# Performance work log

Measured on AMD Instinct MI355X. Metric: run time of the kernel, lower is better.

The kernel has to match this reference:

```python
import jax, jax.numpy as jnp
import numpy as np

DIM = 128        # per-head dim == model width in this module
Q_HEADS = 16
KV_HEADS = 4
WINDOW = 512
BATCH = 4
SEQ = 2048


def setup_inputs() -> dict:
    key = jax.random.key(0)
    k1, k2, k3 = jax.random.split(key, 3)
    x = jax.random.normal(k1, (BATCH, SEQ, DIM), dtype=jnp.float32)
    # fused qkv weight, stored (in, out) so forward is x @ W_qkv
    W_qkv = jax.random.normal(k2, (DIM, (Q_HEADS + 2 * KV_HEADS) * DIM), dtype=jnp.float32) * (DIM ** -0.5)
    W_proj = jax.random.normal(k3, (Q_HEADS * DIM, DIM), dtype=jnp.float32) * ((Q_HEADS * DIM) ** -0.5)
    return {"x": x, "W_qkv": W_qkv, "W_proj": W_proj}


def _gqa_forward(x, W_qkv, W_proj):
    b, s, d = x.shape
    qkv = x @ W_qkv                                    # [b, s, (Hq+2Hkv)*d]
    qkv = qkv.reshape(b, s, Q_HEADS + 2 * KV_HEADS, d).transpose(0, 2, 1, 3)
    q = qkv[:, :Q_HEADS]                               # [b, Hq, s, d]
    k = qkv[:, Q_HEADS:Q_HEADS + KV_HEADS]             # [b, Hkv, s, d]
    v = qkv[:, Q_HEADS + KV_HEADS:]                    # [b, Hkv, s, d]

    # GQA: repeat kv heads to match q heads
    group = Q_HEADS // KV_HEADS
    k = jnp.repeat(k, group, axis=1)                   # [b, Hq, s, d]
    v = jnp.repeat(v, group, axis=1)

    scale = 1.0 / jnp.sqrt(jnp.float32(d))
    scores = jnp.einsum('bhqd,bhkd->bhqk', q, k) * scale   # [b, Hq, s, s]

    q_idx = jnp.arange(s)[:, None]
    kv_idx = jnp.arange(s)[None, :]
    rel = (q_idx - kv_idx).astype(jnp.float32)         # [s, s]
    # per-head ALiBi slope: exp2(-(h+1)*8/Hq), added (sign matches source)
    h = jnp.arange(Q_HEADS, dtype=jnp.float32)
    slopes = jnp.exp2(-((h + 1.0) * 8.0 / Q_HEADS))    # [Hq]
    scores = scores + slopes[None, :, None, None] * rel[None, None, :, :]

    mask = (q_idx >= kv_idx) & ((q_idx - kv_idx) <= WINDOW)
    scores = jnp.where(mask[None, None], scores, -jnp.inf)
    probs = jax.nn.softmax(scores, axis=-1)

    att = jnp.einsum('bhqk,bhkd->bhqd', probs, v)      # [b, Hq, s, d]
    att = att.transpose(0, 2, 1, 3).reshape(b, s, Q_HEADS * d)
    return att @ W_proj                                # [b, s, d]


def reference(x, W_qkv, W_proj):
    return _gqa_forward(x, W_qkv, W_proj)
```

## Files before the change

kernel.cpp:

```cpp
#include <hip/hip_runtime.h>
#include <math.h>

#define DIM_    128
#define QH_     16
#define KVH_    4
#define WIN_    512
#define BATCH_  4
#define SEQ_    2048
#define QKV_LD  3072
#define ATT_LD  2048

#define NX   (BATCH_*SEQ_*DIM_)
#define NWQ  (DIM_*QKV_LD)
#define NWP  (ATT_LD*DIM_)

typedef __attribute__((ext_vector_type(8))) short short8;
typedef __attribute__((ext_vector_type(4))) float f32x4;
typedef unsigned short u16;
typedef unsigned int u32;

__device__ __forceinline__ u16 f2bf(float f) {
    u32 u = __float_as_uint(f);
    u += 0x7fff + ((u >> 16) & 1);
    return (u16)(u >> 16);
}
__device__ __forceinline__ float bf2f(u16 u) {
    return __uint_as_float(((u32)u) << 16);
}
#define MFMA16 __builtin_amdgcn_mfma_f32_16x16x32_bf16

#if __has_builtin(__builtin_amdgcn_exp2f)
#define EXP2F __builtin_amdgcn_exp2f
#else
#define EXP2F exp2f
#endif

__device__ __forceinline__ void gload_lds16(const u16* g, u16* l) {
    __builtin_amdgcn_global_load_lds(
        (const __attribute__((address_space(1))) unsigned int*)(const void*)g,
        (__attribute__((address_space(3))) unsigned int*)(void*)l, 16, 0, 0);
}

__global__ __launch_bounds__(256) void prep(
    const float* __restrict__ x, const float* __restrict__ Wqkv,
    const float* __restrict__ Wproj,
    u16* __restrict__ xh, u16* __restrict__ wth, u16* __restrict__ wpth)
{
    if (blockIdx.x < 1024) {
        const size_t t = (size_t)blockIdx.x * 256 + threadIdx.x;
        float4 v = *(const float4*)(x + 4 * t);
        ushort4 o;
        o.x = f2bf(v.x); o.y = f2bf(v.y); o.z = f2bf(v.z); o.w = f2bf(v.w);
        *(ushort4*)(xh + 4 * t) = o;
        return;
    }
    __shared__ float T[32][33];
    int tile = blockIdx.x - 1024;
    const float* src; u16* dst; int K, N;
    if (tile < 384) { src = Wqkv;  dst = wth;  K = 128;  N = 3072; }
    else { tile -= 384; src = Wproj; dst = wpth; K = 2048; N = 128; }
    const int ntile = N >> 5;
    const int k0 = (tile / ntile) << 5, n0 = (tile % ntile) << 5;
    const int tx = threadIdx.x & 31, ty = threadIdx.x >> 5;
    #pragma unroll
    for (int i = 0; i < 4; ++i)
        T[ty + 8 * i][tx] = src[(size_t)(k0 + ty + 8 * i) * N + n0 + tx];
    __syncthreads();
    #pragma unroll
    for (int i = 0; i < 4; ++i)
        dst[(size_t)(n0 + ty + 8 * i) * K + k0 + tx] = f2bf(T[tx][ty + 8 * i]);
}

__global__ __launch_bounds__(256) void gemm1_mfma(
    const u16* __restrict__ xh, const u16* __restrict__ wth,
    u16* __restrict__ qkvb, u16* __restrict__ vg)
{
    __shared__ u16 Ab[32][512];
    __shared__ u16 Bb[16][512];
    const int bn = blockIdx.x * 64;
    const int bm = blockIdx.y * 128;
    const int tid = threadIdx.x;
    const int wv = tid >> 6, lane = tid & 63;
    const int lr = lane & 15, quad = lane >> 4;
    const int lo = lane & 15, hi = lane >> 4;

    #pragma unroll
    for (int i = 0; i < 12; ++i) {
        const int idx = wv * 12 + i;
        if (idx < 32) {
            const int mt = idx >> 2, s = idx & 3;
            gload_lds16(xh + (size_t)(bm + mt * 16 + lo) * DIM_ + s * 32 + hi * 8,
                        &Ab[idx][0]);
        } else {
            const int j = idx - 32, nt = j >> 2, s = j & 3;
            gload_lds16(wth + (size_t)(bn + nt * 16 + lo) * DIM_ + s * 32 + hi * 8,
                        &Bb[j][0]);
        }
    }
    __syncthreads();

    const int wr = wv >> 1, wc = wv & 1;
    f32x4 acc[4][2] = {};
    if (bn < 2560) {
        #pragma unroll
        for (int s = 0; s < 4; ++s) {
            short8 af[4], bf[2];
            #pragma unroll
            for (int mt = 0; mt < 4; ++mt)
                af[mt] = *(const short8*)&Ab[(wr * 4 + mt) * 4 + s][lane * 8];
            #pragma unroll
            for (int nt = 0; nt < 2; ++nt)
                bf[nt] = *(const short8*)&Bb[(wc * 2 + nt) * 4 + s][lane * 8];
            #pragma unroll
            for (int mt = 0; mt < 4; ++mt)
                #pragma unroll
                for (int nt = 0; nt < 2; ++nt)
                    acc[mt][nt] = MFMA16(bf[nt], af[mt], acc[mt][nt], 0, 0, 0);
        }
        #pragma unroll
        for (int mt = 0; mt < 4; ++mt)
            #pragma unroll
            for (int nt = 0; nt < 2; ++nt) {
                ushort4 o;
                o.x = f2bf(acc[mt][nt][0]); o.y = f2bf(acc[mt][nt][1]);
                o.z = f2bf(acc[mt][nt][2]); o.w = f2bf(acc[mt][nt][3]);
                *(ushort4*)(qkvb
                    + (size_t)(bm + wr * 64 + mt * 16 + lr) * QKV_LD
                    + bn + wc * 32 + nt * 16 + quad * 4) = o;
            }
    } else {
        #pragma unroll
        for (int s = 0; s < 4; ++s) {
            short8 af[4], bf[2];
            #pragma unroll
            for (int mt = 0; mt < 4; ++mt)
                af[mt] = *(const short8*)&Ab[(wr * 4 + mt) * 4 + s][lane * 8];
            #pragma unroll
            for (int nt = 0; nt < 2; ++nt)
                bf[nt] = *(const short8*)&Bb[(wc * 2 + nt) * 4 + s][lane * 8];
            #pragma unroll
            for (int mt = 0; mt < 4; ++mt)
                #pragma unroll
                for (int nt = 0; nt < 2; ++nt)
                    acc[mt][nt] = MFMA16(af[mt], bf[nt], acc[mt][nt], 0, 0, 0);
        }
        #pragma unroll
        for (int mt = 0; mt < 4; ++mt)
            #pragma unroll
            for (int nt = 0; nt < 2; ++nt) {
                const int ncol = bn + wc * 32 + nt * 16 + lr - 2560;
                const int kvh = ncol >> 7, d = ncol & 127;
                const int m0 = bm + wr * 64 + mt * 16 + quad * 4;
                ushort4 o;
                o.x = f2bf(acc[mt][nt][0]); o.y = f2bf(acc[mt][nt][1]);
                o.z = f2bf(acc[mt][nt][2]); o.w = f2bf(acc[mt][nt][3]);
                *(ushort4*)(vg + ((size_t)((m0 >> 11) * KVH_ + kvh) * DIM_ + d)
                            * SEQ_ + (m0 & 2047)) = o;
            }
    }
}

__global__ __launch_bounds__(256) void attn_mfma(
    const u16* __restrict__ qkvb, const u16* __restrict__ vg,
    u16* __restrict__ ah)
{
    const int xcd  = blockIdx.x & 7;
    const int idx  = blockIdx.x >> 3;
    const int pair = xcd + 8 * (idx & 1);
    const int qt   = idx >> 1;
    const int b    = pair >> 2, kvh = pair & 3;
    const int q0 = qt << 5;
    const int tid = threadIdx.x;
    const int wv = tid >> 6, lane = tid & 63;
    const int lr = lane & 15, quad = lane >> 4;
    const int h = kvh * 4 + wv;

    __shared__ u16 Kb[4][8][512];
    __shared__ u16 Vb[4][8][512];
    __shared__ u16 Pt[4][32][36];

    const float scale2 = 0.08838834764831845f * 1.4426950408889634f;
    const float slope2 = exp2f(-0.5f * (float)(h + 1)) * 1.4426950408889634f;
    const int jbase = max(0, q0 - WIN_);
    const int nch = (q0 + 32 - jbase) >> 5;
    const size_t rowb = (size_t)b * SEQ_;
    const u16* kg  = qkvb + rowb * QKV_LD + (QH_ + kvh) * DIM_;
    const u16* vgb = vg + (size_t)(b * KVH_ + kvh) * DIM_ * SEQ_;
    const int lo = lane & 15, hi = lane >> 4;

    short8 qf[2][4];
    #pragma unroll
    for (int m = 0; m < 2; ++m) {
        const u16* qp = qkvb + (rowb + q0 + m * 16 + lr) * QKV_LD
                        + h * DIM_ + quad * 8;
        #pragma unroll
        for (int s = 0; s < 4; ++s) qf[m][s] = *(const short8*)(qp + 32 * s);
    }

    float alpha[2];
    #pragma unroll
    for (int m = 0; m < 2; ++m) {
        const int q = q0 + m * 16 + lr;
        const int rm = (q < WIN_) ? q : WIN_;
        alpha[m] = slope2 * (float)(q - rm);
    }

    f32x4 O[2][8] = {};
    float rs[2] = {0.f, 0.f};

    #define STAGE(CH, SLOT) do {                                              \
        const int _jk = jbase + ((CH) << 5);                                  \
        _Pragma("unroll")                                                     \
        for (int _t = 0; _t < 2; ++_t) {                                      \
            const int _p = wv + _t * 4;                                       \
            gload_lds16(kg + (size_t)(_jk + (_p >> 2) * 16 + lo) * QKV_LD     \
                        + (_p & 3) * 32 + hi * 8, &Kb[(SLOT)][_p][0]);        \
            gload_lds16(vgb + (size_t)(_p * 16 + lo) * SEQ_ + _jk + hi * 8,   \
                        &Vb[(SLOT)][_p][0]);                                  \
        }                                                                     \
    } while (0)

    STAGE(0, 0);
    { const int c1 = (1 < nch) ? 1 : (nch - 1); STAGE(c1, 1); }

    for (int ch = 0; ch < nch; ++ch) {
        const int jk = jbase + (ch << 5);
        const int slot = ch & 3;
        { const int cn = (ch + 2 < nch) ? (ch + 2) : (nch - 1);
          STAGE(cn, (ch + 2) & 3); }
        __asm__ volatile("s_waitcnt vmcnt(8)" ::: "memory");
        __asm__ volatile("s_barrier" ::: "memory");

        #pragma unroll
        for (int nt = 0; nt < 2; ++nt) {
            f32x4 c0 = {0.f, 0.f, 0.f, 0.f}, c1 = {0.f, 0.f, 0.f, 0.f};
            #pragma unroll
            for (int s = 0; s < 4; ++s) {
                short8 kf = *(const short8*)&Kb[slot][nt * 4 + s][lane * 8];
                c0 = MFMA16(kf, qf[0][s], c0, 0, 0, 0);
                c1 = MFMA16(kf, qf[1][s], c1, 0, 0, 0);
            }
            const int jknt = jk + nt * 16;
            #pragma unroll
            for (int m = 0; m < 2; ++m) {
                const f32x4 c = m ? c1 : c0;
                const int qm0 = q0 + m * 16;
                const float b0 = fmaf(-slope2, (float)(jknt + quad * 4), alpha[m]);
                float e0, e1, e2, e3;
                if (qm0 >= jknt + 15 && qm0 + 15 <= jknt + WIN_) {
                    e0 = EXP2F(fmaf(c[0], scale2, b0));
                    e1 = EXP2F(fmaf(c[1], scale2, b0 - slope2));
                    e2 = EXP2F(fmaf(c[2], scale2, b0 - 2.f * slope2));
                    e3 = EXP2F(fmaf(c[3], scale2, b0 - 3.f * slope2));
                } else {
                    const int q = qm0 + lr, j0q = jknt + quad * 4;
                    float ee[4];
                    #pragma unroll
                    for (int r = 0; r < 4; ++r) {
                        const int rel = q - (j0q + r);
                        const float t = fmaf(c[r], scale2, b0 - (float)r * slope2);
                        ee[r] = ((unsigned)rel <= (unsigned)WIN_) ? EXP2F(t) : 0.f;
                    }
                    e0 = ee[0]; e1 = ee[1]; e2 = ee[2]; e3 = ee[3];
                }
                rs[m] += (e0 + e1) + (e2 + e3);
                ushort4 o;
                o.x = f2bf(e0); o.y = f2bf(e1); o.z = f2bf(e2); o.w = f2bf(e3);
                *(ushort4*)&Pt[wv][m * 16 + lr][nt * 16 + quad * 4] = o;
            }
        }
        __asm__ volatile("s_waitcnt lgkmcnt(0)" ::: "memory");

        short8 pa0 = *(const short8*)&Pt[wv][lr][quad * 8];
        short8 pa1 = *(const short8*)&Pt[wv][16 + lr][quad * 8];
        #pragma unroll
        for (int nt = 0; nt < 8; ++nt) {
            short8 vf = *(const short8*)&Vb[slot][nt][lane * 8];
            O[0][nt] = MFMA16(vf, pa0, O[0][nt], 0, 0, 0);
            O[1][nt] = MFMA16(vf, pa1, O[1][nt], 0, 0, 0);
        }
    }
    #undef STAGE

    __asm__ volatile("s_waitcnt vmcnt(0)" ::: "memory");

    #pragma unroll
    for (int m = 0; m < 2; ++m) {
        rs[m] += __shfl_xor(rs[m], 16);
        rs[m] += __shfl_xor(rs[m], 32);
    }

    #pragma unroll
    for (int m = 0; m < 2; ++m) {
        const float inv = 1.0f / rs[m];
        u16* dst = ah + (rowb + q0 + m * 16 + lr) * (size_t)ATT_LD + h * DIM_;
        #pragma unroll
        for (int nt = 0; nt < 8; ++nt) {
            ushort4 o;
            o.x = f2bf(O[m][nt][0] * inv); o.y = f2bf(O[m][nt][1] * inv);
            o.z = f2bf(O[m][nt][2] * inv); o.w = f2bf(O[m][nt][3] * inv);
            *(ushort4*)(dst + nt * 16 + quad * 4) = o;
        }
    }
}

__global__ __launch_bounds__(256) void gemm2_mfma(
    const u16* __restrict__ ah, const u16* __restrict__ wpth,
    float* __restrict__ out)
{
    const int bm = blockIdx.x * 16;
    const int wv = threadIdx.x >> 6, lane = threadIdx.x & 63;
    const int lr = lane & 15, quad = lane >> 4;
    const int cq = wv;

    const u16* arow  = ah + (size_t)(bm + lr) * ATT_LD + quad * 8;
    const u16* w0row = wpth + (size_t)(cq * 32 + lr) * ATT_LD + quad * 8;
    const u16* w1row = w0row + (size_t)16 * ATT_LD;

    f32x4 acc0 = {0.f, 0.f, 0.f, 0.f}, acc1 = {0.f, 0.f, 0.f, 0.f};
    #pragma unroll 8
    for (int k0 = 0; k0 < ATT_LD; k0 += 32) {
        short8 a  = *(const short8*)(arow + k0);
        short8 w0 = *(const short8*)(w0row + k0);
        short8 w1 = *(const short8*)(w1row + k0);
        acc0 = MFMA16(w0, a, acc0, 0, 0, 0);
        acc1 = MFMA16(w1, a, acc1, 0, 0, 0);
    }
    float* orow = out + (size_t)(bm + lr) * DIM_ + cq * 32;
    *(float4*)(orow + quad * 4)      = *(float4*)&acc0;
    *(float4*)(orow + 16 + quad * 4) = *(float4*)&acc1;
}

extern "C" void kernel_launch(void* const* d_in, const int* in_sizes, int n_in,
                              void* d_out, int out_size, void* d_ws, size_t ws_size,
                              hipStream_t stream)
{
    const float* x     = (const float*)d_in[0];
    const float* Wqkv  = (const float*)d_in[1];
    const float* Wproj = (const float*)d_in[2];
    float* out = (float*)d_out;

    u16* xh   = (u16*)d_ws;
    u16* wth  = xh   + (size_t)NX;
    u16* wpth = wth  + (size_t)NWQ;
    u16* qkvb = wpth + (size_t)NWP;
    u16* vg   = qkvb + (size_t)8192 * QKV_LD;
    u16* ahp  = vg   + (size_t)BATCH_ * KVH_ * DIM_ * SEQ_;

    prep<<<1024 + 640, 256, 0, stream>>>(x, Wqkv, Wproj, xh, wth, wpth);

    gemm1_mfma<<<dim3(QKV_LD / 64, 8192 / 128), 256, 0, stream>>>(
        xh, wth, qkvb, vg);

    attn_mfma<<<1024, 256, 0, stream>>>(qkvb, vg, ahp);

    gemm2_mfma<<<8192 / 16, 256, 0, stream>>>(ahp, wpth, out);
}
```

Measured before the change: 202.0 us.

## Shrink attention LDS ring to double buffer, swizzle P tile, use packed bf16 converts

The attention kernel's K/V staging ring drops from four slots to two, and the P tile loses its padding in favour of an XOR swizzle. Together these cut LDS use so more blocks can be resident, and launch bounds now request 4 blocks per CU. A trailing barrier is added to protect slot reuse, and s_setprio raises wave priority around the MFMA bursts. Scalar bf16 rounding is replaced by the hardware v_cvt_pk_bf16_f32 packed convert in all epilogues. The shallower prefetch gives less time to hide load latency, and the extra barrier each chunk adds synchronisation cost.

```diff
diff --git a/kernel.cpp b/kernel.cpp
--- a/kernel.cpp
+++ b/kernel.cpp
@@ -26,6 +26,11 @@
 }
 __device__ __forceinline__ float bf2f(u16 u) {
     return __uint_as_float(((u32)u) << 16);
+}
+__device__ __forceinline__ u32 pkbf(float a, float b) {
+    u32 r;
+    __asm__("v_cvt_pk_bf16_f32 %0, %1, %2" : "=v"(r) : "v"(a), "v"(b));
+    return r;
 }
 #define MFMA16 __builtin_amdgcn_mfma_f32_16x16x32_bf16
 
@@ -121,10 +126,10 @@
         for (int mt = 0; mt < 4; ++mt)
             #pragma unroll
             for (int nt = 0; nt < 2; ++nt) {
-                ushort4 o;
-                o.x = f2bf(acc[mt][nt][0]); o.y = f2bf(acc[mt][nt][1]);
-                o.z = f2bf(acc[mt][nt][2]); o.w = f2bf(acc[mt][nt][3]);
-                *(ushort4*)(qkvb
+                uint2 o;
+                o.x = pkbf(acc[mt][nt][0], acc[mt][nt][1]);
+                o.y = pkbf(acc[mt][nt][2], acc[mt][nt][3]);
+                *(uint2*)(qkvb
                     + (size_t)(bm + wr * 64 + mt * 16 + lr) * QKV_LD
                     + bn + wc * 32 + nt * 16 + quad * 4) = o;
             }
@@ -151,16 +156,16 @@
                 const int ncol = bn + wc * 32 + nt * 16 + lr - 2560;
                 const int kvh = ncol >> 7, d = ncol & 127;
                 const int m0 = bm + wr * 64 + mt * 16 + quad * 4;
-                ushort4 o;
-                o.x = f2bf(acc[mt][nt][0]); o.y = f2bf(acc[mt][nt][1]);
-                o.z = f2bf(acc[mt][nt][2]); o.w = f2bf(acc[mt][nt][3]);
-                *(ushort4*)(vg + ((size_t)((m0 >> 11) * KVH_ + kvh) * DIM_ + d)
+                uint2 o;
+                o.x = pkbf(acc[mt][nt][0], acc[mt][nt][1]);
+                o.y = pkbf(acc[mt][nt][2], acc[mt][nt][3]);
+                *(uint2*)(vg + ((size_t)((m0 >> 11) * KVH_ + kvh) * DIM_ + d)
                             * SEQ_ + (m0 & 2047)) = o;
             }
     }
 }
 
-__global__ __launch_bounds__(256) void attn_mfma(
+__global__ __launch_bounds__(256, 4) void attn_mfma(
     const u16* __restrict__ qkvb, const u16* __restrict__ vg,
     u16* __restrict__ ah)
 {
@@ -174,10 +179,11 @@
     const int wv = tid >> 6, lane = tid & 63;
     const int lr = lane & 15, quad = lane >> 4;
     const int h = kvh * 4 + wv;
-
-    __shared__ u16 Kb[4][8][512];
-    __shared__ u16 Vb[4][8][512];
-    __shared__ u16 Pt[4][32][36];
+    const int key3 = ((lr >> 1) & 3) << 3;
+
+    __shared__ u16 Kb[2][8][512];
+    __shared__ u16 Vb[2][8][512];
+    __shared__ u16 Pt[4][32][32];
 
     const float scale2 = 0.08838834764831845f * 1.4426950408889634f;
     const float slope2 = exp2f(-0.5f * (float)(h + 1)) * 1.4426950408889634f;
@@ -221,25 +227,26 @@
     } while (0)
 
     STAGE(0, 0);
-    { const int c1 = (1 < nch) ? 1 : (nch - 1); STAGE(c1, 1); }
 
     for (int ch = 0; ch < nch; ++ch) {
         const int jk = jbase + (ch << 5);
-        const int slot = ch & 3;
-        { const int cn = (ch + 2 < nch) ? (ch + 2) : (nch - 1);
-          STAGE(cn, (ch + 2) & 3); }
-        __asm__ volatile("s_waitcnt vmcnt(8)" ::: "memory");
+        const int slot = ch & 1;
+        { const int cn = (ch + 1 < nch) ? (ch + 1) : (nch - 1);
+          STAGE(cn, slot ^ 1); }
+        __asm__ volatile("s_waitcnt vmcnt(4)" ::: "memory");
         __asm__ volatile("s_barrier" ::: "memory");
 
         #pragma unroll
         for (int nt = 0; nt < 2; ++nt) {
             f32x4 c0 = {0.f, 0.f, 0.f, 0.f}, c1 = {0.f, 0.f, 0.f, 0.f};
+            __builtin_amdgcn_s_setprio(1);
             #pragma unroll
             for (int s = 0; s < 4; ++s) {
                 short8 kf = *(const short8*)&Kb[slot][nt * 4 + s][lane * 8];
                 c0 = MFMA16(kf, qf[0][s], c0, 0, 0, 0);
                 c1 = MFMA16(kf, qf[1][s], c1, 0, 0, 0);
             }
+            __builtin_amdgcn_s_setprio(0);
             const int jknt = jk + nt * 16;
             #pragma unroll
             for (int m = 0; m < 2; ++m) {
@@ -264,21 +271,25 @@
                     e0 = ee[0]; e1 = ee[1]; e2 = ee[2]; e3 = ee[3];
                 }
                 rs[m] += (e0 + e1) + (e2 + e3);
-                ushort4 o;
-                o.x = f2bf(e0); o.y = f2bf(e1); o.z = f2bf(e2); o.w = f2bf(e3);
-                *(ushort4*)&Pt[wv][m * 16 + lr][nt * 16 + quad * 4] = o;
+                uint2 o;
+                o.x = pkbf(e0, e1);
+                o.y = pkbf(e2, e3);
+                *(uint2*)&Pt[wv][m * 16 + lr][(nt * 16 + quad * 4) ^ key3] = o;
             }
         }
         __asm__ volatile("s_waitcnt lgkmcnt(0)" ::: "memory");
 
-        short8 pa0 = *(const short8*)&Pt[wv][lr][quad * 8];
-        short8 pa1 = *(const short8*)&Pt[wv][16 + lr][quad * 8];
+        short8 pa0 = *(const short8*)&Pt[wv][lr][(quad * 8) ^ key3];
+        short8 pa1 = *(const short8*)&Pt[wv][16 + lr][(quad * 8) ^ key3];
+        __builtin_amdgcn_s_setprio(1);
         #pragma unroll
         for (int nt = 0; nt < 8; ++nt) {
             short8 vf = *(const short8*)&Vb[slot][nt][lane * 8];
             O[0][nt] = MFMA16(vf, pa0, O[0][nt], 0, 0, 0);
             O[1][nt] = MFMA16(vf, pa1, O[1][nt], 0, 0, 0);
         }
+        __builtin_amdgcn_s_setprio(0);
+        __asm__ volatile("s_barrier" ::: "memory");
     }
     #undef STAGE
 
@@ -296,10 +307,10 @@
         u16* dst = ah + (rowb + q0 + m * 16 + lr) * (size_t)ATT_LD + h * DIM_;
         #pragma unroll
         for (int nt = 0; nt < 8; ++nt) {
-            ushort4 o;
-            o.x = f2bf(O[m][nt][0] * inv); o.y = f2bf(O[m][nt][1] * inv);
-            o.z = f2bf(O[m][nt][2] * inv); o.w = f2bf(O[m][nt][3] * inv);
-            *(ushort4*)(dst + nt * 16 + quad * 4) = o;
+            uint2 o;
+            o.x = pkbf(O[m][nt][0] * inv, O[m][nt][1] * inv);
+            o.y = pkbf(O[m][nt][2] * inv, O[m][nt][3] * inv);
+            *(uint2*)(dst + nt * 16 + quad * 4) = o;
         }
     }
 }
```

Result: slower. 263.1 us (+30.3%).
